# Performance work log

Measured on AMD Instinct MI355X. Metric: run time of the kernel, lower is better.

Reference implementation:

```python
import jax, jax.numpy as jnp
import numpy as np

N_HEADS = 16
N_KV_HEADS = 4
HEAD_DIM = 128


def _rope(x, cos, sin):
    # x: [b, s, h, d]; cos/sin: [s, d//2]; interleaved pair rotation
    b, s, h, d = x.shape
    xp = x.reshape(b, s, h, d // 2, 2)
    x_r, x_i = xp[..., 0], xp[..., 1]
    c = cos[None, :, None, :]
    sn = sin[None, :, None, :]
    o_r = x_r * c - x_i * sn
    o_i = x_r * sn + x_i * c
    return jnp.stack([o_r, o_i], axis=-1).reshape(b, s, h, d)


def setup_inputs() -> dict:
    key = jax.random.key(0)
    ks = jax.random.split(key, 7)
    B, S, D = 2, 2048, 2048
    KV = N_KV_HEADS * HEAD_DIM
    x = jax.random.normal(ks[0], (B, S, D), dtype=jnp.float32)
    freqs_cos = jax.random.uniform(ks[1], (S, HEAD_DIM // 2), dtype=jnp.float32)
    freqs_sin = jax.random.uniform(ks[2], (S, HEAD_DIM // 2), dtype=jnp.float32)
    scale = 0.02
    wq = jax.random.normal(ks[3], (D, D), dtype=jnp.float32) * scale
    wk = jax.random.normal(ks[4], (KV, D), dtype=jnp.float32) * scale
    wv = jax.random.normal(ks[5], (KV, D), dtype=jnp.float32) * scale
    wo = jax.random.normal(ks[6], (D, D), dtype=jnp.float32) * scale
    return {"x": x, "freqs_cos": freqs_cos, "freqs_sin": freqs_sin,
            "wq": wq, "wk": wk, "wv": wv, "wo": wo}


def reference(x, freqs_cos, freqs_sin, wq, wk, wv, wo):
    B, S, D = x.shape
    n_rep = N_HEADS // N_KV_HEADS
    q = (x @ wq.T).reshape(B, S, N_HEADS, HEAD_DIM)
    k = (x @ wk.T).reshape(B, S, N_KV_HEADS, HEAD_DIM)
    v = (x @ wv.T).reshape(B, S, N_KV_HEADS, HEAD_DIM)
    q = _rope(q, freqs_cos, freqs_sin)
    k = _rope(k, freqs_cos, freqs_sin)
    # repeat_kv == torch.repeat_interleave along head dim
    k = jnp.repeat(k, n_rep, axis=2)
    v = jnp.repeat(v, n_rep, axis=2)
    q = q.transpose(0, 2, 1, 3)  # [B, H, S, d]
    k = k.transpose(0, 2, 1, 3)
    v = v.transpose(0, 2, 1, 3)
    scale = 1.0 / np.sqrt(HEAD_DIM).astype(np.float32)
    scores = jnp.einsum('bhqd,bhkd->bhqk', q, k) * scale
    causal = jnp.tril(jnp.ones((S, S), dtype=bool))
    scores = jnp.where(causal[None, None], scores, jnp.finfo(jnp.float32).min)
    probs = jax.nn.softmax(scores.astype(jnp.float32), axis=-1).astype(q.dtype)
    out = jnp.einsum('bhqk,bhkd->bhqd', probs, v)
    out = out.transpose(0, 2, 1, 3).reshape(B, S, N_HEADS * HEAD_DIM)
    return out @ wo.T
```

## Files before the change

### kernel.cpp

```cpp
#include <hip/hip_runtime.h>
#include <hip/hip_bf16.h>
#include <type_traits>

using bf16x8 = __attribute__((ext_vector_type(8))) short;
using f32x4  = __attribute__((ext_vector_type(4))) float;
using u16x8  = __attribute__((ext_vector_type(8))) unsigned short;
using u32x4  = __attribute__((ext_vector_type(4))) unsigned int;

__device__ __forceinline__ float b2f(unsigned short u) {
    unsigned int x = ((unsigned int)u) << 16;
    return __builtin_bit_cast(float, x);
}
__device__ __forceinline__ unsigned short f2b(float f) {
    __hip_bfloat16 h = __float2bfloat16(f);
    return __builtin_bit_cast(unsigned short, h);
}

__device__ __forceinline__ void async_copy16(const void* g, void* l) {
    __builtin_amdgcn_global_load_lds(
        (const __attribute__((address_space(1))) unsigned int*)g,
        (__attribute__((address_space(3))) unsigned int*)l, 16, 0, 0);
}

#define MFMA16(a, b, c) __builtin_amdgcn_mfma_f32_16x16x32_bf16(a, b, c, 0, 0, 0)

__global__ __launch_bounds__(256) void cvt_f32_to_bf16(
    const float* __restrict__ s, unsigned short* __restrict__ d, int n4)
{
    int i = blockIdx.x * blockDim.x + threadIdx.x;
    if (i >= n4) return;
    float4 v = ((const float4*)s)[i];
    ushort4 o;
    o.x = f2b(v.x); o.y = f2b(v.y); o.z = f2b(v.z); o.w = f2b(v.w);
    ((ushort4*)d)[i] = o;
}

__global__ __launch_bounds__(256) void qkv_gemm(
    const unsigned short* __restrict__ A,
    const unsigned short* __restrict__ Wq,
    const unsigned short* __restrict__ Wk,
    const unsigned short* __restrict__ Wv,
    unsigned short* __restrict__ Q,
    unsigned short* __restrict__ Kk,
    unsigned short* __restrict__ V)
{
    const int K = 2048;
    constexpr int BK = 64;
    __shared__ unsigned short As[128 * BK];
    __shared__ unsigned short Bs[128 * BK];

    int tid  = threadIdx.x;
    int w    = tid >> 6;
    int lane = tid & 63;
    int idx  = lane & 15;
    int quad = lane >> 4;
    int wm   = (w >> 1) * 64;
    int wn   = (w & 1) * 64;

    int bm = blockIdx.x / 24;
    int bn = blockIdx.x - bm * 24;
    int m0 = bm * 128;

    const unsigned short* Bt;
    unsigned short* C;
    int Nc, n0;
    if (bn < 16)      { Bt = Wq + (size_t)bn * 128 * K;        C = Q;  Nc = 2048; n0 = bn * 128; }
    else if (bn < 20) { Bt = Wk + (size_t)(bn - 16) * 128 * K; C = Kk; Nc = 512;  n0 = (bn - 16) * 128; }
    else              { Bt = Wv + (size_t)(bn - 20) * 128 * K; C = V;  Nc = 512;  n0 = (bn - 20) * 128; }

    int srow   = lane >> 3;
    int schunk = (lane & 7) ^ srow;

    f32x4 acc[4][4];
    #pragma unroll
    for (int mi = 0; mi < 4; ++mi)
        #pragma unroll
        for (int ni = 0; ni < 4; ++ni) acc[mi][ni] = (f32x4){0.f, 0.f, 0.f, 0.f};

    for (int k0 = 0; k0 < K; k0 += BK) {
        #pragma unroll
        for (int i = 0; i < 4; ++i) {
            int cb = w * 4 + i;
            size_t goff = (size_t)(cb * 8 + srow) * K + k0 + schunk * 8;
            async_copy16(A + (size_t)m0 * K + goff, &As[cb * 512]);
            async_copy16(Bt + goff, &Bs[cb * 512]);
        }
        __syncthreads();

        #pragma unroll
        for (int ks = 0; ks < 2; ++ks) {
            bf16x8 af[4], bfr[4];
            #pragma unroll
            for (int mi = 0; mi < 4; ++mi) {
                int row = wm + mi * 16 + idx;
                af[mi] = *(const bf16x8*)&As[row * BK + (((ks * 4 + quad) ^ (row & 7)) * 8)];
            }
            #pragma unroll
            for (int ni = 0; ni < 4; ++ni) {
                int row = wn + ni * 16 + idx;
                bfr[ni] = *(const bf16x8*)&Bs[row * BK + (((ks * 4 + quad) ^ (row & 7)) * 8)];
            }
            #pragma unroll
            for (int mi = 0; mi < 4; ++mi)
                #pragma unroll
                for (int ni = 0; ni < 4; ++ni)
                    acc[mi][ni] = MFMA16(af[mi], bfr[ni], acc[mi][ni]);
        }
        __syncthreads();
    }

    #pragma unroll
    for (int mi = 0; mi < 4; ++mi) {
        #pragma unroll
        for (int r = 0; r < 4; ++r) {
            size_t row = (size_t)(m0 + wm + mi * 16 + quad * 4 + r);
            #pragma unroll
            for (int ni = 0; ni < 4; ++ni) {
                int col = n0 + wn + ni * 16 + idx;
                C[row * Nc + col] = f2b(acc[mi][ni][r]);
            }
        }
    }
}

template <typename OutT>
__global__ __launch_bounds__(256) void gemm_tile(
    const unsigned short* __restrict__ A,
    const unsigned short* __restrict__ Bt,
    OutT* __restrict__ C,
    int M, int N, int K)
{
    constexpr int BK = 64;
    __shared__ unsigned short As[128 * BK];
    __shared__ unsigned short Bs[128 * BK];

    int tid  = threadIdx.x;
    int w    = tid >> 6;
    int lane = tid & 63;
    int idx  = lane & 15;
    int quad = lane >> 4;
    int wm   = (w >> 1) * 64;
    int wn   = (w & 1) * 64;

    int tilesN = N / 128;
    int bm = blockIdx.x / tilesN;
    int bn = blockIdx.x - bm * tilesN;
    int m0 = bm * 128, n0 = bn * 128;

    int srow   = lane >> 3;
    int schunk = (lane & 7) ^ srow;

    f32x4 acc[4][4];
    #pragma unroll
    for (int mi = 0; mi < 4; ++mi)
        #pragma unroll
        for (int ni = 0; ni < 4; ++ni) acc[mi][ni] = (f32x4){0.f, 0.f, 0.f, 0.f};

    for (int k0 = 0; k0 < K; k0 += BK) {
        #pragma unroll
        for (int i = 0; i < 4; ++i) {
            int cb = w * 4 + i;
            size_t goff = (size_t)(cb * 8 + srow) * K + k0 + schunk * 8;
            async_copy16(A  + (size_t)m0 * K + goff, &As[cb * 512]);
            async_copy16(Bt + (size_t)n0 * K + goff, &Bs[cb * 512]);
        }
        __syncthreads();

        #pragma unroll
        for (int ks = 0; ks < 2; ++ks) {
            bf16x8 af[4], bfr[4];
            #pragma unroll
            for (int mi = 0; mi < 4; ++mi) {
                int row = wm + mi * 16 + idx;
                af[mi] = *(const bf16x8*)&As[row * BK + (((ks * 4 + quad) ^ (row & 7)) * 8)];
            }
            #pragma unroll
            for (int ni = 0; ni < 4; ++ni) {
                int row = wn + ni * 16 + idx;
                bfr[ni] = *(const bf16x8*)&Bs[row * BK + (((ks * 4 + quad) ^ (row & 7)) * 8)];
            }
            #pragma unroll
            for (int mi = 0; mi < 4; ++mi)
                #pragma unroll
                for (int ni = 0; ni < 4; ++ni)
                    acc[mi][ni] = MFMA16(af[mi], bfr[ni], acc[mi][ni]);
        }
        __syncthreads();
    }

    #pragma unroll
    for (int mi = 0; mi < 4; ++mi) {
        #pragma unroll
        for (int r = 0; r < 4; ++r) {
            size_t row = (size_t)(m0 + wm + mi * 16 + quad * 4 + r);
            #pragma unroll
            for (int ni = 0; ni < 4; ++ni) {
                int col = n0 + wn + ni * 16 + idx;
                if constexpr (std::is_same_v<OutT, float>) {
                    C[row * N + col] = acc[mi][ni][r];
                } else {
                    C[row * N + col] = f2b(acc[mi][ni][r]);
                }
            }
        }
    }
}

__global__ __launch_bounds__(256) void rope_kernel(
    unsigned short* __restrict__ x,
    const float* __restrict__ cs,
    const float* __restrict__ sn,
    int H, int total, float oscale)
{
    int e = blockIdx.x * blockDim.x + threadIdx.x;
    if (e >= total) return;
    int i = e & 63;
    int s = (e / (64 * H)) & 2047;
    float xr = b2f(x[2 * e]);
    float xi = b2f(x[2 * e + 1]);
    float c  = cs[s * 64 + i];
    float sv = sn[s * 64 + i];
    x[2 * e]     = f2b((xr * c - xi * sv) * oscale);
    x[2 * e + 1] = f2b((xr * sv + xi * c) * oscale);
}

__global__ __launch_bounds__(256) void flash_attn(
    const unsigned short* __restrict__ q,
    const unsigned short* __restrict__ kk,
    const unsigned short* __restrict__ vv,
    unsigned short* __restrict__ out)
{
    const int S = 2048;
    int bid = blockIdx.x;
    int qp  = bid & 15;
    int bh  = bid >> 4;
    int h   = bh & 15;
    int b   = bh >> 4;
    int kvh = h >> 2;

    int tid  = threadIdx.x;
    int w    = tid >> 6;
    int lane = tid & 63;
    int idx  = lane & 15;
    int quad = lane >> 4;

    __shared__ unsigned short Ks[32 * 128];
    __shared__ unsigned short Vt[128 * 40];

    const unsigned short* kbase = kk + ((size_t)b * S * 4 + kvh) * 128;
    const unsigned short* vbase = vv + ((size_t)b * S * 4 + kvh) * 128;

    int dp = (tid & 63) * 2;
    int jb = tid >> 6;

    for (int phase = 0; phase < 2; ++phase) {
        int qt  = phase ? (31 - qp) : qp;
        int q0  = qt * 64;
        int wq0 = q0 + w * 16;
        int qr  = wq0 + idx;

        bf16x8 qf[4];
        {
            const unsigned short* qpp =
                q + ((size_t)((b * S + wq0 + idx) * 16 + h)) * 128 + quad * 8;
            #pragma unroll
            for (int ko = 0; ko < 4; ++ko)
                qf[ko] = *(const bf16x8*)(qpp + ko * 32);
        }

        f32x4 acc[8];
        #pragma unroll
        for (int n = 0; n < 8; ++n) acc[n] = (f32x4){0.f, 0.f, 0.f, 0.f};
        float lsum = 0.f;

        int ntiles = (q0 + 64) >> 5;
        for (int t = 0; t < ntiles; ++t) {
            #pragma unroll
            for (int it = 0; it < 2; ++it) {
                int i   = w * 2 + it;
                int key = i * 4 + (lane >> 4);
                int sc  = (lane & 15) ^ (key & 7);
                async_copy16(kbase + ((size_t)(t * 32 + key)) * 512 + sc * 8,
                             &Ks[i * 512]);
            }
            {
                const unsigned short* vc =
                    vbase + ((size_t)(t * 32 + jb * 4)) * 512 + dp;
                unsigned int ld[8];
                #pragma unroll
                for (int i = 0; i < 8; ++i) {
                    int key = (i >> 1) + 16 * (i & 1);
                    ld[i] = *(const unsigned int*)(vc + key * 512);
                }
                u16x8 lo, hi;
                #pragma unroll
                for (int i = 0; i < 8; ++i) {
                    lo[i] = (unsigned short)ld[i];
                    hi[i] = (unsigned short)(ld[i] >> 16);
                }
                *(u16x8*)&Vt[dp * 40 + jb * 8]       = lo;
                *(u16x8*)&Vt[(dp + 1) * 40 + jb * 8] = hi;
            }
            __syncthreads();

            if (t * 32 <= wq0 + 15) {
                f32x4 s0 = {0.f,0.f,0.f,0.f}, s1 = {0.f,0.f,0.f,0.f};
                #pragma unroll
                for (int ko = 0; ko < 4; ++ko) {
                    int kc = ko * 4 + quad;
                    bf16x8 kf0 = *(const bf16x8*)&Ks[idx * 128 + ((kc ^ (idx & 7)) * 8)];
                    bf16x8 kf1 = *(const bf16x8*)&Ks[(16 + idx) * 128 + ((kc ^ (idx & 7)) * 8)];
                    s0 = MFMA16(kf0, qf[ko], s0);
                    s1 = MFMA16(kf1, qf[ko], s1);
                }
                int L = qr - t * 32;
                unsigned int pk[4];
                #pragma unroll
                for (int r = 0; r < 4; ++r) {
                    int kl = quad * 4 + r;
                    float p0 = (kl      <= L) ? exp2f(s0[r]) : 0.f;
                    float p1 = (kl + 16 <= L) ? exp2f(s1[r]) : 0.f;
                    lsum += p0 + p1;
                    pk[r] = (unsigned int)f2b(p0) | ((unsigned int)f2b(p1) << 16);
                }
                u32x4 pku = {pk[0], pk[1], pk[2], pk[3]};
                bf16x8 pf = __builtin_bit_cast(bf16x8, pku);
                #pragma unroll
                for (int n = 0; n < 8; ++n) {
                    bf16x8 vf = *(const bf16x8*)&Vt[(n * 16 + idx) * 40 + quad * 8];
                    acc[n] = MFMA16(vf, pf, acc[n]);
                }
            }
            __syncthreads();
        }

        lsum += __shfl_xor(lsum, 16);
        lsum += __shfl_xor(lsum, 32);
        float inv = 1.f / lsum;
        size_t rowb = (size_t)(b * S + wq0 + idx) * 2048 + h * 128;
        #pragma unroll
        for (int n = 0; n < 8; ++n) {
            ushort4 o;
            o.x = f2b(acc[n][0] * inv);
            o.y = f2b(acc[n][1] * inv);
            o.z = f2b(acc[n][2] * inv);
            o.w = f2b(acc[n][3] * inv);
            *(ushort4*)&out[rowb + n * 16 + quad * 4] = o;
        }
    }
}

extern "C" void kernel_launch(void* const* d_in, const int* in_sizes, int n_in,
                              void* d_out, int out_size, void* d_ws, size_t ws_size,
                              hipStream_t stream)
{
    const float* x  = (const float*)d_in[0];
    const float* fc = (const float*)d_in[1];
    const float* fs = (const float*)d_in[2];
    const float* wq = (const float*)d_in[3];
    const float* wk = (const float*)d_in[4];
    const float* wv = (const float*)d_in[5];
    const float* wo = (const float*)d_in[6];
    float* out = (float*)d_out;

    const int B = 2, S = 2048, D = 2048, KV = 512;
    const int M = B * S;

    unsigned short* ws  = (unsigned short*)d_ws;
    unsigned short* xb  = ws;
    unsigned short* wqb = xb  + (size_t)M * D;
    unsigned short* wkb = wqb + (size_t)D * D;
    unsigned short* wvb = wkb + (size_t)KV * D;
    unsigned short* wob = wvb + (size_t)KV * D;
    unsigned short* qb  = wob + (size_t)D * D;
    unsigned short* kb  = qb  + (size_t)M * D;
    unsigned short* vb  = kb  + (size_t)M * KV;
    unsigned short* ao  = vb  + (size_t)M * KV;

    cvt_f32_to_bf16<<<dim3((M * D / 4) / 256), dim3(256), 0, stream>>>(x,  xb,  M * D / 4);
    cvt_f32_to_bf16<<<dim3((D * D / 4) / 256), dim3(256), 0, stream>>>(wq, wqb, D * D / 4);
    cvt_f32_to_bf16<<<dim3((KV * D / 4) / 256), dim3(256), 0, stream>>>(wk, wkb, KV * D / 4);
    cvt_f32_to_bf16<<<dim3((KV * D / 4) / 256), dim3(256), 0, stream>>>(wv, wvb, KV * D / 4);
    cvt_f32_to_bf16<<<dim3((D * D / 4) / 256), dim3(256), 0, stream>>>(wo, wob, D * D / 4);

    qkv_gemm<<<dim3(768), dim3(256), 0, stream>>>(xb, wqb, wkb, wvb, qb, kb, vb);

    int qpairs = B * S * 16 * 64;
    int kpairs = B * S * 4 * 64;
    const float c2 = 0.12752584f;
    rope_kernel<<<dim3(qpairs / 256), dim3(256), 0, stream>>>(qb, fc, fs, 16, qpairs, c2);
    rope_kernel<<<dim3(kpairs / 256), dim3(256), 0, stream>>>(kb, fc, fs, 4, kpairs, 1.0f);

    flash_attn<<<dim3(512), dim3(256), 0, stream>>>(qb, kb, vb, ao);

    gemm_tile<float><<<dim3((M / 128) * (D / 128)), dim3(256), 0, stream>>>(ao, wob, out, M, D, D);
}
```

Measured before the change: 340.8 us.

## Double-buffer K/V tiles and give each wave two query row blocks in flash attention

Restructures the attention kernel so K/V tiles are double-buffered in shared memory: the next tile's K is issued asynchronously and its V loaded into registers while the current tile is computed, leaving one barrier per iteration instead of two. Blocks shrink to 2 waves that each handle 32 query rows (two 16-row blocks), so every K and V fragment read from LDS feeds twice as many MFMAs. The grid doubles to 1024 blocks, each taking one query tile instead of a balanced pair. Full unmasked tiles take a fast path without per-element mask checks. The cost is higher register pressure and twice the LDS per block.

```diff
diff --git a/kernel.cpp b/kernel.cpp
--- a/kernel.cpp
+++ b/kernel.cpp
@@ -224,127 +224,191 @@
     x[2 * e + 1] = f2b((xr * sv + xi * c) * oscale);
 }
 
-__global__ __launch_bounds__(256) void flash_attn(
-    const unsigned short* __restrict__ q,
+__global__ __launch_bounds__(128, 2) void flash_attn(
+    const unsigned short* __restrict__ qg,
     const unsigned short* __restrict__ kk,
     const unsigned short* __restrict__ vv,
     unsigned short* __restrict__ out)
 {
     const int S = 2048;
     int bid = blockIdx.x;
-    int qp  = bid & 15;
-    int bh  = bid >> 4;
+    int qp  = bid & 31;
+    int bh  = bid >> 5;
     int h   = bh & 15;
     int b   = bh >> 4;
     int kvh = h >> 2;
+    int qt  = (qp & 1) ? (31 - (qp >> 1)) : (qp >> 1);
+    int q0  = qt * 64;
 
     int tid  = threadIdx.x;
     int w    = tid >> 6;
     int lane = tid & 63;
     int idx  = lane & 15;
     int quad = lane >> 4;
-
-    __shared__ unsigned short Ks[32 * 128];
-    __shared__ unsigned short Vt[128 * 40];
+    int wq0  = q0 + w * 32;
+
+    __shared__ unsigned short Ks[2][32 * 128];
+    __shared__ unsigned short Vt[2][128 * 40];
 
     const unsigned short* kbase = kk + ((size_t)b * S * 4 + kvh) * 128;
     const unsigned short* vbase = vv + ((size_t)b * S * 4 + kvh) * 128;
 
-    int dp = (tid & 63) * 2;
-    int jb = tid >> 6;
-
-    for (int phase = 0; phase < 2; ++phase) {
-        int qt  = phase ? (31 - qp) : qp;
-        int q0  = qt * 64;
-        int wq0 = q0 + w * 16;
-        int qr  = wq0 + idx;
-
-        bf16x8 qf[4];
-        {
-            const unsigned short* qpp =
-                q + ((size_t)((b * S + wq0 + idx) * 16 + h)) * 128 + quad * 8;
-            #pragma unroll
-            for (int ko = 0; ko < 4; ++ko)
-                qf[ko] = *(const bf16x8*)(qpp + ko * 32);
-        }
-
-        f32x4 acc[8];
-        #pragma unroll
-        for (int n = 0; n < 8; ++n) acc[n] = (f32x4){0.f, 0.f, 0.f, 0.f};
-        float lsum = 0.f;
-
-        int ntiles = (q0 + 64) >> 5;
-        for (int t = 0; t < ntiles; ++t) {
-            #pragma unroll
-            for (int it = 0; it < 2; ++it) {
-                int i   = w * 2 + it;
+    bf16x8 qf[2][4];
+    #pragma unroll
+    for (int rb = 0; rb < 2; ++rb) {
+        const unsigned short* qpp =
+            qg + ((size_t)((b * S + wq0 + rb * 16 + idx) * 16 + h)) * 128 + quad * 8;
+        #pragma unroll
+        for (int ko = 0; ko < 4; ++ko)
+            qf[rb][ko] = *(const bf16x8*)(qpp + ko * 32);
+    }
+
+    f32x4 acc[2][8];
+    #pragma unroll
+    for (int rb = 0; rb < 2; ++rb)
+        #pragma unroll
+        for (int n = 0; n < 8; ++n) acc[rb][n] = (f32x4){0.f, 0.f, 0.f, 0.f};
+    float lsum[2] = {0.f, 0.f};
+
+    int nt = 2 * qt + 2;
+
+    int dp  = (tid & 63) * 2;
+    int jb0 = (tid >> 6) * 2;
+    unsigned int vld[2][8];
+
+    #pragma unroll
+    for (int it = 0; it < 4; ++it) {
+        int i   = w * 4 + it;
+        int key = i * 4 + (lane >> 4);
+        int sc  = (lane & 15) ^ (key & 7);
+        async_copy16(kbase + (size_t)key * 512 + sc * 8, &Ks[0][i * 512]);
+    }
+    #pragma unroll
+    for (int m = 0; m < 2; ++m) {
+        const unsigned short* vc = vbase + ((size_t)(jb0 + m) * 4) * 512 + dp;
+        #pragma unroll
+        for (int i = 0; i < 8; ++i) {
+            int key = (i >> 1) + 16 * (i & 1);
+            vld[m][i] = *(const unsigned int*)(vc + key * 512);
+        }
+    }
+    #pragma unroll
+    for (int m = 0; m < 2; ++m) {
+        u16x8 lo, hi;
+        #pragma unroll
+        for (int i = 0; i < 8; ++i) {
+            lo[i] = (unsigned short)vld[m][i];
+            hi[i] = (unsigned short)(vld[m][i] >> 16);
+        }
+        *(u16x8*)&Vt[0][dp * 40 + (jb0 + m) * 8]       = lo;
+        *(u16x8*)&Vt[0][(dp + 1) * 40 + (jb0 + m) * 8] = hi;
+    }
+
+    for (int t = 0; t < nt; ++t) {
+        int buf = t & 1;
+        __syncthreads();
+
+        if (t + 1 < nt) {
+            int nbuf = buf ^ 1;
+            #pragma unroll
+            for (int it = 0; it < 4; ++it) {
+                int i   = w * 4 + it;
                 int key = i * 4 + (lane >> 4);
                 int sc  = (lane & 15) ^ (key & 7);
-                async_copy16(kbase + ((size_t)(t * 32 + key)) * 512 + sc * 8,
-                             &Ks[i * 512]);
-            }
-            {
+                async_copy16(kbase + ((size_t)((t + 1) * 32 + key)) * 512 + sc * 8,
+                             &Ks[nbuf][i * 512]);
+            }
+            #pragma unroll
+            for (int m = 0; m < 2; ++m) {
                 const unsigned short* vc =
-                    vbase + ((size_t)(t * 32 + jb * 4)) * 512 + dp;
-                unsigned int ld[8];
+                    vbase + ((size_t)((t + 1) * 32 + (jb0 + m) * 4)) * 512 + dp;
                 #pragma unroll
                 for (int i = 0; i < 8; ++i) {
                     int key = (i >> 1) + 16 * (i & 1);
-                    ld[i] = *(const unsigned int*)(vc + key * 512);
+                    vld[m][i] = *(const unsigned int*)(vc + key * 512);
                 }
+            }
+        }
+
+        if (t * 32 <= wq0 + 31) {
+            f32x4 s00 = {0.f,0.f,0.f,0.f}, s01 = {0.f,0.f,0.f,0.f};
+            f32x4 s10 = {0.f,0.f,0.f,0.f}, s11 = {0.f,0.f,0.f,0.f};
+            #pragma unroll
+            for (int ko = 0; ko < 4; ++ko) {
+                int kc = ko * 4 + quad;
+                bf16x8 kf0 = *(const bf16x8*)&Ks[buf][idx * 128 + ((kc ^ (idx & 7)) * 8)];
+                bf16x8 kf1 = *(const bf16x8*)&Ks[buf][(16 + idx) * 128 + ((kc ^ (idx & 7)) * 8)];
+                s00 = MFMA16(kf0, qf[0][ko], s00);
+                s01 = MFMA16(kf1, qf[0][ko], s01);
+                s10 = MFMA16(kf0, qf[1][ko], s10);
+                s11 = MFMA16(kf1, qf[1][ko], s11);
+            }
+            bf16x8 pf[2];
+            #pragma unroll
+            for (int rb = 0; rb < 2; ++rb) {
+                f32x4 sa = rb ? s10 : s00;
+                f32x4 sb = rb ? s11 : s01;
+                unsigned int pk[4];
+                if (t * 32 + 31 <= wq0 + rb * 16) {
+                    #pragma unroll
+                    for (int r = 0; r < 4; ++r) {
+                        float p0 = exp2f(sa[r]);
+                        float p1 = exp2f(sb[r]);
+                        lsum[rb] += p0 + p1;
+                        pk[r] = (unsigned int)f2b(p0) | ((unsigned int)f2b(p1) << 16);
+                    }
+                } else {
+                    int L = wq0 + rb * 16 + idx - t * 32;
+                    #pragma unroll
+                    for (int r = 0; r < 4; ++r) {
+                        int kl = quad * 4 + r;
+                        float p0 = (kl      <= L) ? exp2f(sa[r]) : 0.f;
+                        float p1 = (kl + 16 <= L) ? exp2f(sb[r]) : 0.f;
+                        lsum[rb] += p0 + p1;
+                        pk[r] = (unsigned int)f2b(p0) | ((unsigned int)f2b(p1) << 16);
+                    }
+                }
+                u32x4 pku = {pk[0], pk[1], pk[2], pk[3]};
+                pf[rb] = __builtin_bit_cast(bf16x8, pku);
+            }
+            #pragma unroll
+            for (int n = 0; n < 8; ++n) {
+                bf16x8 vf = *(const bf16x8*)&Vt[buf][(n * 16 + idx) * 40 + quad * 8];
+                acc[0][n] = MFMA16(vf, pf[0], acc[0][n]);
+                acc[1][n] = MFMA16(vf, pf[1], acc[1][n]);
+            }
+        }
+
+        if (t + 1 < nt) {
+            int nbuf = buf ^ 1;
+            #pragma unroll
+            for (int m = 0; m < 2; ++m) {
                 u16x8 lo, hi;
                 #pragma unroll
                 for (int i = 0; i < 8; ++i) {
-                    lo[i] = (unsigned short)ld[i];
-                    hi[i] = (unsigned short)(ld[i] >> 16);
+                    lo[i] = (unsigned short)vld[m][i];
+                    hi[i] = (unsigned short)(vld[m][i] >> 16);
                 }
-                *(u16x8*)&Vt[dp * 40 + jb * 8]       = lo;
-                *(u16x8*)&Vt[(dp + 1) * 40 + jb * 8] = hi;
-            }
-            __syncthreads();
-
-            if (t * 32 <= wq0 + 15) {
-                f32x4 s0 = {0.f,0.f,0.f,0.f}, s1 = {0.f,0.f,0.f,0.f};
-                #pragma unroll
-                for (int ko = 0; ko < 4; ++ko) {
-                    int kc = ko * 4 + quad;
-                    bf16x8 kf0 = *(const bf16x8*)&Ks[idx * 128 + ((kc ^ (idx & 7)) * 8)];
-                    bf16x8 kf1 = *(const bf16x8*)&Ks[(16 + idx) * 128 + ((kc ^ (idx & 7)) * 8)];
-                    s0 = MFMA16(kf0, qf[ko], s0);
-                    s1 = MFMA16(kf1, qf[ko], s1);
-                }
-                int L = qr - t * 32;
-                unsigned int pk[4];
-                #pragma unroll
-                for (int r = 0; r < 4; ++r) {
-                    int kl = quad * 4 + r;
-                    float p0 = (kl      <= L) ? exp2f(s0[r]) : 0.f;
-                    float p1 = (kl + 16 <= L) ? exp2f(s1[r]) : 0.f;
-                    lsum += p0 + p1;
-                    pk[r] = (unsigned int)f2b(p0) | ((unsigned int)f2b(p1) << 16);
-                }
-                u32x4 pku = {pk[0], pk[1], pk[2], pk[3]};
-                bf16x8 pf = __builtin_bit_cast(bf16x8, pku);
-                #pragma unroll
-                for (int n = 0; n < 8; ++n) {
-                    bf16x8 vf = *(const bf16x8*)&Vt[(n * 16 + idx) * 40 + quad * 8];
-                    acc[n] = MFMA16(vf, pf, acc[n]);
-                }
-            }
-            __syncthreads();
-        }
-
-        lsum += __shfl_xor(lsum, 16);
-        lsum += __shfl_xor(lsum, 32);
-        float inv = 1.f / lsum;
-        size_t rowb = (size_t)(b * S + wq0 + idx) * 2048 + h * 128;
+                *(u16x8*)&Vt[nbuf][dp * 40 + (jb0 + m) * 8]       = lo;
+                *(u16x8*)&Vt[nbuf][(dp + 1) * 40 + (jb0 + m) * 8] = hi;
+            }
+        }
+    }
+
+    #pragma unroll
+    for (int rb = 0; rb < 2; ++rb) {
+        float ls = lsum[rb];
+        ls += __shfl_xor(ls, 16);
+        ls += __shfl_xor(ls, 32);
+        float inv = 1.f / ls;
+        size_t rowb = (size_t)(b * S + wq0 + rb * 16 + idx) * 2048 + h * 128;
         #pragma unroll
         for (int n = 0; n < 8; ++n) {
             ushort4 o;
-            o.x = f2b(acc[n][0] * inv);
-            o.y = f2b(acc[n][1] * inv);
-            o.z = f2b(acc[n][2] * inv);
-            o.w = f2b(acc[n][3] * inv);
+            o.x = f2b(acc[rb][n][0] * inv);
+            o.y = f2b(acc[rb][n][1] * inv);
+            o.z = f2b(acc[rb][n][2] * inv);
+            o.w = f2b(acc[rb][n][3] * inv);
             *(ushort4*)&out[rowb + n * 16 + quad * 4] = o;
         }
     }
@@ -391,7 +455,7 @@
     rope_kernel<<<dim3(qpairs / 256), dim3(256), 0, stream>>>(qb, fc, fs, 16, qpairs, c2);
     rope_kernel<<<dim3(kpairs / 256), dim3(256), 0, stream>>>(kb, fc, fs, 4, kpairs, 1.0f);
 
-    flash_attn<<<dim3(512), dim3(256), 0, stream>>>(qb, kb, vb, ao);
+    flash_attn<<<dim3(1024), dim3(128), 0, stream>>>(qb, kb, vb, ao);
 
     gemm_tile<float><<<dim3((M / 128) * (D / 128)), dim3(256), 0, stream>>>(ao, wob, out, M, D, D);
 }
```

Measured after the change: 359.7 us. 1.06x slower.

## Run both causal q-tile phases concurrently in one 512-thread block with shared K/V tiles

Applied to the files above, without the earlier changes.

The flash attention block grows from 256 to 512 threads. The two paired query tiles (qp and 31-qp), which were processed one after the other, now run at the same time in separate wave groups. K/V tiles are loaded once per key step and shared by both halves, which cuts redundant K/V loads and the serial phase loop. It also adds a fast path that skips causal masking for tiles lying fully below the diagonal. In exchange, the waves on the short tile sit idle at barriers while the long tile finishes, and per-block register pressure rises.

```diff
diff --git a/kernel.cpp b/kernel.cpp
--- a/kernel.cpp
+++ b/kernel.cpp
@@ -5,6 +5,7 @@
 using bf16x8 = __attribute__((ext_vector_type(8))) short;
 using f32x4  = __attribute__((ext_vector_type(4))) float;
 using u16x8  = __attribute__((ext_vector_type(8))) unsigned short;
+using u16x4  = __attribute__((ext_vector_type(4))) unsigned short;
 using u32x4  = __attribute__((ext_vector_type(4))) unsigned int;
 
 __device__ __forceinline__ float b2f(unsigned short u) {
@@ -224,8 +225,8 @@
     x[2 * e + 1] = f2b((xr * sv + xi * c) * oscale);
 }
 
-__global__ __launch_bounds__(256) void flash_attn(
-    const unsigned short* __restrict__ q,
+__global__ __launch_bounds__(512, 4) void flash_attn(
+    const unsigned short* __restrict__ qg,
     const unsigned short* __restrict__ kk,
     const unsigned short* __restrict__ vv,
     unsigned short* __restrict__ out)
@@ -244,77 +245,86 @@
     int idx  = lane & 15;
     int quad = lane >> 4;
 
+    int qt  = (w >> 2) ? (31 - qp) : qp;
+    int q0  = qt * 64;
+    int wq0 = q0 + (w & 3) * 16;
+    int qr  = wq0 + idx;
+
     __shared__ unsigned short Ks[32 * 128];
     __shared__ unsigned short Vt[128 * 40];
 
     const unsigned short* kbase = kk + ((size_t)b * S * 4 + kvh) * 128;
     const unsigned short* vbase = vv + ((size_t)b * S * 4 + kvh) * 128;
 
+    bf16x8 qf[4];
+    {
+        const unsigned short* qpp =
+            qg + ((size_t)((b * S + wq0 + idx) * 16 + h)) * 128 + quad * 8;
+        #pragma unroll
+        for (int ko = 0; ko < 4; ++ko)
+            qf[ko] = *(const bf16x8*)(qpp + ko * 32);
+    }
+
+    f32x4 acc[8];
+    #pragma unroll
+    for (int n = 0; n < 8; ++n) acc[n] = (f32x4){0.f, 0.f, 0.f, 0.f};
+    float lsum = 0.f;
+
     int dp = (tid & 63) * 2;
-    int jb = tid >> 6;
-
-    for (int phase = 0; phase < 2; ++phase) {
-        int qt  = phase ? (31 - qp) : qp;
-        int q0  = qt * 64;
-        int wq0 = q0 + w * 16;
-        int qr  = wq0 + idx;
-
-        bf16x8 qf[4];
+    int jb = (tid >> 6) & 3;
+    int ih = (tid >> 8) * 4;
+
+    int ntA = 2 * qp + 2, ntB = 64 - 2 * qp;
+    int nt  = ntA > ntB ? ntA : ntB;
+
+    for (int t = 0; t < nt; ++t) {
         {
-            const unsigned short* qpp =
-                q + ((size_t)((b * S + wq0 + idx) * 16 + h)) * 128 + quad * 8;
-            #pragma unroll
-            for (int ko = 0; ko < 4; ++ko)
-                qf[ko] = *(const bf16x8*)(qpp + ko * 32);
-        }
-
-        f32x4 acc[8];
-        #pragma unroll
-        for (int n = 0; n < 8; ++n) acc[n] = (f32x4){0.f, 0.f, 0.f, 0.f};
-        float lsum = 0.f;
-
-        int ntiles = (q0 + 64) >> 5;
-        for (int t = 0; t < ntiles; ++t) {
-            #pragma unroll
-            for (int it = 0; it < 2; ++it) {
-                int i   = w * 2 + it;
-                int key = i * 4 + (lane >> 4);
-                int sc  = (lane & 15) ^ (key & 7);
-                async_copy16(kbase + ((size_t)(t * 32 + key)) * 512 + sc * 8,
-                             &Ks[i * 512]);
-            }
-            {
-                const unsigned short* vc =
-                    vbase + ((size_t)(t * 32 + jb * 4)) * 512 + dp;
-                unsigned int ld[8];
+            int key = w * 4 + (lane >> 4);
+            int sc  = (lane & 15) ^ (key & 7);
+            async_copy16(kbase + ((size_t)(t * 32 + key)) * 512 + sc * 8,
+                         &Ks[w * 512]);
+        }
+        {
+            const unsigned short* vc = vbase + ((size_t)(t * 32 + jb * 4)) * 512 + dp;
+            unsigned int ld[4];
+            #pragma unroll
+            for (int i = 0; i < 4; ++i) {
+                int ii  = ih + i;
+                int key = (ii >> 1) + 16 * (ii & 1);
+                ld[i] = *(const unsigned int*)(vc + key * 512);
+            }
+            u16x4 lo, hi;
+            #pragma unroll
+            for (int i = 0; i < 4; ++i) {
+                lo[i] = (unsigned short)ld[i];
+                hi[i] = (unsigned short)(ld[i] >> 16);
+            }
+            *(u16x4*)&Vt[dp * 40 + jb * 8 + ih]       = lo;
+            *(u16x4*)&Vt[(dp + 1) * 40 + jb * 8 + ih] = hi;
+        }
+        __syncthreads();
+
+        if (t * 32 <= wq0 + 15) {
+            f32x4 s0 = {0.f,0.f,0.f,0.f}, s1 = {0.f,0.f,0.f,0.f};
+            #pragma unroll
+            for (int ko = 0; ko < 4; ++ko) {
+                int kc = ko * 4 + quad;
+                bf16x8 kf0 = *(const bf16x8*)&Ks[idx * 128 + ((kc ^ (idx & 7)) * 8)];
+                bf16x8 kf1 = *(const bf16x8*)&Ks[(16 + idx) * 128 + ((kc ^ (idx & 7)) * 8)];
+                s0 = MFMA16(kf0, qf[ko], s0);
+                s1 = MFMA16(kf1, qf[ko], s1);
+            }
+            unsigned int pk[4];
+            if (t * 32 + 31 <= wq0) {
                 #pragma unroll
-                for (int i = 0; i < 8; ++i) {
-                    int key = (i >> 1) + 16 * (i & 1);
-                    ld[i] = *(const unsigned int*)(vc + key * 512);
+                for (int r = 0; r < 4; ++r) {
+                    float p0 = exp2f(s0[r]);
+                    float p1 = exp2f(s1[r]);
+                    lsum += p0 + p1;
+                    pk[r] = (unsigned int)f2b(p0) | ((unsigned int)f2b(p1) << 16);
                 }
-                u16x8 lo, hi;
-                #pragma unroll
-                for (int i = 0; i < 8; ++i) {
-                    lo[i] = (unsigned short)ld[i];
-                    hi[i] = (unsigned short)(ld[i] >> 16);
-                }
-                *(u16x8*)&Vt[dp * 40 + jb * 8]       = lo;
-                *(u16x8*)&Vt[(dp + 1) * 40 + jb * 8] = hi;
-            }
-            __syncthreads();
-
-            if (t * 32 <= wq0 + 15) {
-                f32x4 s0 = {0.f,0.f,0.f,0.f}, s1 = {0.f,0.f,0.f,0.f};
-                #pragma unroll
-                for (int ko = 0; ko < 4; ++ko) {
-                    int kc = ko * 4 + quad;
-                    bf16x8 kf0 = *(const bf16x8*)&Ks[idx * 128 + ((kc ^ (idx & 7)) * 8)];
-                    bf16x8 kf1 = *(const bf16x8*)&Ks[(16 + idx) * 128 + ((kc ^ (idx & 7)) * 8)];
-                    s0 = MFMA16(kf0, qf[ko], s0);
-                    s1 = MFMA16(kf1, qf[ko], s1);
-                }
+            } else {
                 int L = qr - t * 32;
-                unsigned int pk[4];
                 #pragma unroll
                 for (int r = 0; r < 4; ++r) {
                     int kl = quad * 4 + r;
@@ -323,30 +333,30 @@
                     lsum += p0 + p1;
                     pk[r] = (unsigned int)f2b(p0) | ((unsigned int)f2b(p1) << 16);
                 }
-                u32x4 pku = {pk[0], pk[1], pk[2], pk[3]};
-                bf16x8 pf = __builtin_bit_cast(bf16x8, pku);
-                #pragma unroll
-                for (int n = 0; n < 8; ++n) {
-                    bf16x8 vf = *(const bf16x8*)&Vt[(n * 16 + idx) * 40 + quad * 8];
-                    acc[n] = MFMA16(vf, pf, acc[n]);
-                }
-            }
-            __syncthreads();
-        }
-
-        lsum += __shfl_xor(lsum, 16);
-        lsum += __shfl_xor(lsum, 32);
-        float inv = 1.f / lsum;
-        size_t rowb = (size_t)(b * S + wq0 + idx) * 2048 + h * 128;
-        #pragma unroll
-        for (int n = 0; n < 8; ++n) {
-            ushort4 o;
-            o.x = f2b(acc[n][0] * inv);
-            o.y = f2b(acc[n][1] * inv);
-            o.z = f2b(acc[n][2] * inv);
-            o.w = f2b(acc[n][3] * inv);
-            *(ushort4*)&out[rowb + n * 16 + quad * 4] = o;
-        }
+            }
+            u32x4 pku = {pk[0], pk[1], pk[2], pk[3]};
+            bf16x8 pf = __builtin_bit_cast(bf16x8, pku);
+            #pragma unroll
+            for (int n = 0; n < 8; ++n) {
+                bf16x8 vf = *(const bf16x8*)&Vt[(n * 16 + idx) * 40 + quad * 8];
+                acc[n] = MFMA16(vf, pf, acc[n]);
+            }
+        }
+        __syncthreads();
+    }
+
+    lsum += __shfl_xor(lsum, 16);
+    lsum += __shfl_xor(lsum, 32);
+    float inv = 1.f / lsum;
+    size_t rowb = (size_t)(b * S + wq0 + idx) * 2048 + h * 128;
+    #pragma unroll
+    for (int n = 0; n < 8; ++n) {
+        ushort4 o;
+        o.x = f2b(acc[n][0] * inv);
+        o.y = f2b(acc[n][1] * inv);
+        o.z = f2b(acc[n][2] * inv);
+        o.w = f2b(acc[n][3] * inv);
+        *(ushort4*)&out[rowb + n * 16 + quad * 4] = o;
     }
 }
 
@@ -391,7 +401,7 @@
     rope_kernel<<<dim3(qpairs / 256), dim3(256), 0, stream>>>(qb, fc, fs, 16, qpairs, c2);
     rope_kernel<<<dim3(kpairs / 256), dim3(256), 0, stream>>>(kb, fc, fs, 4, kpairs, 1.0f);
 
-    flash_attn<<<dim3(512), dim3(256), 0, stream>>>(qb, kb, vb, ao);
+    flash_attn<<<dim3(512), dim3(512), 0, stream>>>(qb, kb, vb, ao);
 
     gemm_tile<float><<<dim3((M / 128) * (D / 128)), dim3(256), 0, stream>>>(ao, wob, out, M, D, D);
 }
```

Measured after the change: 338.8 us. Within noise of the previous version (-0.6%).
